# Kernel tuning notes

Hardware: AMD Instinct MI355X
Metric: run time of the kernel (lower is better)

The kernel has to match this reference:

```python
import jax, jax.numpy as jnp
import numpy as np

D = 1024
H = 16
HD = D // H
EPS = 1e-5

def _layernorm(x, g, b):
    xf = x.astype(jnp.float32)
    mu = jnp.mean(xf, axis=-1, keepdims=True)
    var = jnp.mean(jnp.square(xf - mu), axis=-1, keepdims=True)
    return ((xf - mu) * jax.lax.rsqrt(var + EPS) * g + b).astype(x.dtype)

def setup_inputs() -> dict:
    key = jax.random.key(0)
    ks = jax.random.split(key, 12)
    B, S = 4, 1024
    s_in = 1.0 / np.sqrt(D)
    inp = {
        "x": jax.random.normal(ks[0], (B, S, D), dtype=jnp.float32),
        "in_proj_w": jax.random.normal(ks[1], (3 * D, D), dtype=jnp.float32) * s_in,
        "in_proj_b": jnp.zeros((3 * D,), dtype=jnp.float32),
        "out_w": jax.random.normal(ks[2], (D, D), dtype=jnp.float32) * s_in,
        "out_b": jnp.zeros((D,), dtype=jnp.float32),
        "ln1_g": jnp.ones((D,), dtype=jnp.float32),
        "ln1_b": jnp.zeros((D,), dtype=jnp.float32),
        "fc_w": jax.random.normal(ks[3], (4 * D, D), dtype=jnp.float32) * s_in,
        "fc_b": jnp.zeros((4 * D,), dtype=jnp.float32),
        "proj_w": jax.random.normal(ks[4], (D, 4 * D), dtype=jnp.float32) * (1.0 / np.sqrt(4 * D)),
        "proj_b": jnp.zeros((D,), dtype=jnp.float32),
        "ln2_g": jnp.ones((D,), dtype=jnp.float32),
        "ln2_b": jnp.zeros((D,), dtype=jnp.float32),
    }
    return inp

def reference(x, in_proj_w, in_proj_b, out_w, out_b, ln1_g, ln1_b,
              fc_w, fc_b, proj_w, proj_b, ln2_g, ln2_b):
    B, S, _ = x.shape
    scaling = float(HD) ** -0.5
    # --- attention sublayer ---
    h = _layernorm(x, ln1_g, ln1_b)
    qkv = h @ in_proj_w.T + in_proj_b              # [B,S,3D]
    q, k, v = jnp.split(qkv, 3, axis=-1)
    q = (q * scaling).reshape(B, S, H, HD).transpose(0, 2, 1, 3)  # [B,H,S,hd]
    k = k.reshape(B, S, H, HD).transpose(0, 2, 1, 3)
    v = v.reshape(B, S, H, HD).transpose(0, 2, 1, 3)
    attn = jax.nn.softmax(jnp.einsum('bhqd,bhkd->bhqk', q, k), axis=-1)
    o = jnp.einsum('bhqk,bhkd->bhqd', attn, v).transpose(0, 2, 1, 3).reshape(B, S, D)
    x = x + o @ out_w.T + out_b
    # --- MLP sublayer (QuickGELU) ---
    h = _layernorm(x, ln2_g, ln2_b)
    u = h @ fc_w.T + fc_b                          # [B,S,4D]
    u = u * jax.nn.sigmoid(1.702 * u)
    x = x + u @ proj_w.T + proj_b
    return x
```

## Files before the change

### kernel.cpp

```cpp
#include <hip/hip_runtime.h>
#include <math.h>

#define D_MODEL 1024
#define SEQ     1024
#define BATCH   4
#define NTOK    (BATCH * SEQ)

typedef __bf16 bf16;
using bfrag  = __attribute__((ext_vector_type(8))) __bf16;
using ffrag  = __attribute__((ext_vector_type(4))) float;
using f32x16 = __attribute__((ext_vector_type(16))) float;

__device__ __forceinline__ ffrag mfma16(bfrag a, bfrag b, ffrag c) {
  return __builtin_amdgcn_mfma_f32_16x16x32_bf16(a, b, c, 0, 0, 0);
}
__device__ __forceinline__ f32x16 mfma32(bfrag a, bfrag b, f32x16 c) {
  return __builtin_amdgcn_mfma_f32_32x32x16_bf16(a, b, c, 0, 0, 0);
}
__device__ __forceinline__ unsigned cvt_pk(float lo, float hi) {
  unsigned r;
  asm("v_cvt_pk_bf16_f32 %0, %1, %2" : "=v"(r) : "v"(lo), "v"(hi));
  return r;
}

__device__ __forceinline__ void gload_lds16(const void* g, void* l) {
  __builtin_amdgcn_global_load_lds(
      (const __attribute__((address_space(1))) void*)g,
      (__attribute__((address_space(3))) void*)l, 16, 0, 0);
}

__device__ __forceinline__ int xcd_remap(int flat, int nwg) {
  return (flat & 7) * (nwg >> 3) + (flat >> 3);
}

__global__ void convert_all(const float* __restrict__ s0, bf16* __restrict__ d0, int n0,
                            const float* __restrict__ s1, bf16* __restrict__ d1, int n1,
                            const float* __restrict__ s2, bf16* __restrict__ d2, int n2,
                            const float* __restrict__ s3, bf16* __restrict__ d3, int n3,
                            float scale, int limit0) {
  const float* src; bf16* dst; int n; int limit = 0;
  switch (blockIdx.y) {
    case 0: src = s0; dst = d0; n = n0; limit = limit0; break;
    case 1: src = s1; dst = d1; n = n1; break;
    case 2: src = s2; dst = d2; n = n2; break;
    default: src = s3; dst = d3; n = n3; break;
  }
  int i = blockIdx.x * blockDim.x + threadIdx.x;
  const int stride = gridDim.x * blockDim.x;
  for (; i < n; i += stride) {
    float4 v = ((const float4*)src)[i];
    float sc = (i < limit) ? scale : 1.0f;
    bf16* d = dst + (size_t)i * 4;
    d[0] = (bf16)(v.x * sc); d[1] = (bf16)(v.y * sc);
    d[2] = (bf16)(v.z * sc); d[3] = (bf16)(v.w * sc);
  }
}

__global__ void scale_bias(const float* __restrict__ src, float* __restrict__ dst,
                           int n, int limit, float scale) {
  int i = blockIdx.x * blockDim.x + threadIdx.x;
  if (i < n) dst[i] = src[i] * (i < limit ? scale : 1.0f);
}

__global__ __launch_bounds__(256) void ln_row(const float* __restrict__ x,
                                              const float* __restrict__ gamma,
                                              const float* __restrict__ beta,
                                              bf16* __restrict__ out) {
  const int row = blockIdx.x, tid = threadIdx.x;
  const float4 v = ((const float4*)(x + (size_t)row * D_MODEL))[tid];
  float s  = v.x + v.y + v.z + v.w;
  float ss = v.x * v.x + v.y * v.y + v.z * v.z + v.w * v.w;
#pragma unroll
  for (int off = 32; off >= 1; off >>= 1) {
    s  += __shfl_xor(s, off);
    ss += __shfl_xor(ss, off);
  }
  __shared__ float rs[4], rss[4];
  const int w = tid >> 6;
  if ((tid & 63) == 0) { rs[w] = s; rss[w] = ss; }
  __syncthreads();
  s  = rs[0] + rs[1] + rs[2] + rs[3];
  ss = rss[0] + rss[1] + rss[2] + rss[3];
  const float mu   = s * (1.0f / D_MODEL);
  const float var  = ss * (1.0f / D_MODEL) - mu * mu;
  const float rstd = rsqrtf(var + 1e-5f);
  const float4 gv = ((const float4*)gamma)[tid];
  const float4 bv = ((const float4*)beta)[tid];
  bf16* o = out + (size_t)row * D_MODEL + tid * 4;
  o[0] = (bf16)((v.x - mu) * rstd * gv.x + bv.x);
  o[1] = (bf16)((v.y - mu) * rstd * gv.y + bv.y);
  o[2] = (bf16)((v.z - mu) * rstd * gv.z + bv.z);
  o[3] = (bf16)((v.w - mu) * rstd * gv.w + bv.w);
}

template <int EPI>
__global__ __launch_bounds__(256, 4) void gemm_bt(
    const bf16* __restrict__ A, const bf16* __restrict__ B,
    const float* __restrict__ bias, const float* __restrict__ resid,
    float* __restrict__ outF, bf16* __restrict__ outB,
    int M, int N, int K) {
  __shared__ bf16 As[2][128 * 32];
  __shared__ bf16 Bs[2][128 * 32];
  const int tid = threadIdx.x;
  const int lane = tid & 63, w = tid >> 6;
  const int wm = w >> 1, wn = w & 1;
  const int ql = lane & 15, lg = lane >> 4;
  const int nwg = gridDim.x * gridDim.y;
  const int flat = xcd_remap(blockIdx.y * gridDim.x + blockIdx.x, nwg);
  const int m0 = (flat % gridDim.x) * 128, n0 = (flat / gridDim.x) * 128;

  ffrag acc[4][4];
#pragma unroll
  for (int i = 0; i < 4; i++)
#pragma unroll
    for (int j = 0; j < 4; j++) acc[i][j] = ffrag{0.f, 0.f, 0.f, 0.f};

  const int r0 = tid >> 2;
  const int jsw = (tid & 3) ^ ((r0 >> 1) & 3);
  const bf16* a0 = A + (size_t)(m0 + r0) * K + jsw * 8;
  const bf16* a1 = A + (size_t)(m0 + 64 + r0) * K + jsw * 8;
  const bf16* b0 = B + (size_t)(n0 + r0) * K + jsw * 8;
  const bf16* b1 = B + (size_t)(n0 + 64 + r0) * K + jsw * 8;
  const int lo = w * 512;

  auto STAGE = [&](int bs, int kk) {
    gload_lds16(a0 + kk, &As[bs][lo]);
    gload_lds16(a1 + kk, &As[bs][2048 + lo]);
    gload_lds16(b0 + kk, &Bs[bs][lo]);
    gload_lds16(b1 + kk, &Bs[bs][2048 + lo]);
  };

  STAGE(0, 0);
  __syncthreads();

  int cur = 0;
  for (int k0 = 0; k0 < K; k0 += 32) {
    if (k0 + 32 < K) STAGE(cur ^ 1, k0 + 32);
    bfrag af[4], bfr[4];
#pragma unroll
    for (int i = 0; i < 4; i++) {
      const int row = wm * 64 + i * 16 + ql;
      af[i] = *(const bfrag*)&As[cur][row * 32 + ((lg ^ ((row >> 1) & 3)) * 8)];
    }
#pragma unroll
    for (int j = 0; j < 4; j++) {
      const int row = wn * 64 + j * 16 + ql;
      bfr[j] = *(const bfrag*)&Bs[cur][row * 32 + ((lg ^ ((row >> 1) & 3)) * 8)];
    }
#pragma unroll
    for (int i = 0; i < 4; i++)
#pragma unroll
      for (int j = 0; j < 4; j++)
        acc[i][j] = mfma16(af[i], bfr[j], acc[i][j]);
    __syncthreads();
    cur ^= 1;
  }

#pragma unroll
  for (int i = 0; i < 4; i++) {
    const int row = m0 + wm * 64 + i * 16 + lg * 4;
#pragma unroll
    for (int j = 0; j < 4; j++) {
      const int col = n0 + wn * 64 + j * 16 + ql;
      const float bv = bias[col];
#pragma unroll
      for (int r = 0; r < 4; r++) {
        float v = acc[i][j][r] + bv;
        const size_t idx = (size_t)(row + r) * N + col;
        if (EPI == 0) {
          outB[idx] = (bf16)v;
        } else if (EPI == 1) {
          outF[idx] = v + resid[idx];
        } else {
          outB[idx] = (bf16)(v / (1.0f + __expf(-1.702f * v)));
        }
      }
    }
  }
}

template <int EPI>
__global__ __launch_bounds__(256, 4) void gemm_bt64(
    const bf16* __restrict__ A, const bf16* __restrict__ B,
    const float* __restrict__ bias, const float* __restrict__ resid,
    float* __restrict__ outF, bf16* __restrict__ outB,
    int M, int N, int K) {
  __shared__ bf16 As[2][64 * 64];
  __shared__ bf16 Bs[2][64 * 64];
  const int tid = threadIdx.x;
  const int lane = tid & 63, w = tid >> 6;
  const int wm = w >> 1, wn = w & 1;
  const int ql = lane & 15, lg = lane >> 4;
  const int bid = blockIdx.x;
  const int k8 = bid & 7, j8 = bid >> 3;
  const int m0 = (k8 * 8 + (j8 & 7)) * 64;
  const int n0 = (j8 >> 3) * 64;

  ffrag acc[2][2];
#pragma unroll
  for (int i = 0; i < 2; i++)
#pragma unroll
    for (int j = 0; j < 2; j++) acc[i][j] = ffrag{0.f, 0.f, 0.f, 0.f};

  const int r0 = tid >> 3;
  const int jsw = ((tid & 7) ^ (r0 & 7)) * 8;
  const bf16* a0 = A + (size_t)(m0 + r0) * K + jsw;
  const bf16* a1 = A + (size_t)(m0 + 32 + r0) * K + jsw;
  const bf16* b0 = B + (size_t)(n0 + r0) * K + jsw;
  const bf16* b1 = B + (size_t)(n0 + 32 + r0) * K + jsw;
  const int lo = tid * 8;

  auto STAGE = [&](int bs, int kk) {
    gload_lds16(a0 + kk, &As[bs][lo]);
    gload_lds16(a1 + kk, &As[bs][2048 + lo]);
    gload_lds16(b0 + kk, &Bs[bs][lo]);
    gload_lds16(b1 + kk, &Bs[bs][2048 + lo]);
  };

  STAGE(0, 0);
  __syncthreads();

  int cur = 0;
  for (int k0 = 0; k0 < K; k0 += 64) {
    if (k0 + 64 < K) STAGE(cur ^ 1, k0 + 64);
    bfrag af[2][2], bfr[2][2];
#pragma unroll
    for (int i = 0; i < 2; i++) {
      const int row = wm * 32 + i * 16 + ql;
      const int r7 = row & 7;
#pragma unroll
      for (int kc = 0; kc < 2; kc++)
        af[i][kc] = *(const bfrag*)&As[cur][row * 64 + (((lg + 4 * kc) ^ r7) * 8)];
    }
#pragma unroll
    for (int j = 0; j < 2; j++) {
      const int row = wn * 32 + j * 16 + ql;
      const int r7 = row & 7;
#pragma unroll
      for (int kc = 0; kc < 2; kc++)
        bfr[j][kc] = *(const bfrag*)&Bs[cur][row * 64 + (((lg + 4 * kc) ^ r7) * 8)];
    }
#pragma unroll
    for (int kc = 0; kc < 2; kc++)
#pragma unroll
      for (int i = 0; i < 2; i++)
#pragma unroll
        for (int j = 0; j < 2; j++)
          acc[i][j] = mfma16(af[i][kc], bfr[j][kc], acc[i][j]);
    __syncthreads();
    cur ^= 1;
  }

#pragma unroll
  for (int i = 0; i < 2; i++) {
    const int row = m0 + wm * 32 + i * 16 + lg * 4;
#pragma unroll
    for (int j = 0; j < 2; j++) {
      const int col = n0 + wn * 32 + j * 16 + ql;
      const float bv = bias[col];
#pragma unroll
      for (int r = 0; r < 4; r++) {
        float v = acc[i][j][r] + bv;
        const size_t idx = (size_t)(row + r) * N + col;
        if (EPI == 0) {
          outB[idx] = (bf16)v;
        } else if (EPI == 1) {
          outF[idx] = v + resid[idx];
        } else {
          outB[idx] = (bf16)(v / (1.0f + __expf(-1.702f * v)));
        }
      }
    }
  }
}

__global__ __launch_bounds__(256) void transpose_v(const bf16* __restrict__ qkv,
                                                   bf16* __restrict__ vt) {
  __shared__ bf16 T[64 * 66];
  const int tid = threadIdx.x;
  const int bh = blockIdx.y, b = bh >> 4, h = bh & 15;
  const int s0 = blockIdx.x * 64;
  const bf16* src = qkv + (size_t)b * SEQ * 3072 + 2048 + h * 64;

  const int sl = tid >> 3, c = tid & 7;
#pragma unroll
  for (int p = 0; p < 2; p++) {
    const int s = sl + p * 32;
    const bfrag v = *(const bfrag*)(src + (size_t)(s0 + s) * 3072 + c * 8);
#pragma unroll
    for (int e = 0; e < 8; e++) T[s * 66 + c * 8 + e] = v[e];
  }
  __syncthreads();
  bf16* dst = vt + (size_t)bh * 64 * 1024;
#pragma unroll
  for (int p = 0; p < 2; p++) {
    const int d = sl + p * 32;
    bfrag o;
#pragma unroll
    for (int e = 0; e < 8; e++) o[e] = T[(c * 8 + e) * 66 + d];
    *(bfrag*)(dst + (size_t)d * 1024 + s0 + c * 8) = o;
  }
}

__global__ __launch_bounds__(256, 2) void flash_attn(const bf16* __restrict__ qkv,
                                                     const bf16* __restrict__ vt,
                                                     bf16* __restrict__ o) {
  __shared__ bf16 Kl[128 * 64];
  __shared__ bf16 Vl[64 * 128];
  __shared__ float RB[4][32];
  const int tid = threadIdx.x, lane = tid & 63, wid = tid >> 6;
  const int l31 = lane & 31, hi = lane >> 5;
  const int flat = xcd_remap(blockIdx.y * 8 + blockIdx.x, 512);
  const int qblk = flat & 7, bh = flat >> 3, b = bh >> 4, h = bh & 15;
  const int qb0 = qblk * 128 + wid * 32;
  const size_t headq = (size_t)b * SEQ * 3072 + (size_t)h * 64;

  const bf16* qp = qkv + headq + (size_t)(qb0 + l31) * 3072 + hi * 8;
  bfrag qb[4];
#pragma unroll
  for (int t = 0; t < 4; t++) qb[t] = *(const bfrag*)(qp + t * 16);

  float mrun = -1e30f, lrun = 0.0f;
  f32x16 oacc[2];
#pragma unroll
  for (int r = 0; r < 16; r++) { oacc[0][r] = 0.f; oacc[1][r] = 0.f; }

  const int ksrc = ((tid & 7) ^ ((tid >> 3) & 7) ^ wid) * 8;
  const bf16* kp = qkv + headq + 1024 + (size_t)(tid >> 3) * 3072 + ksrc;
  const bf16* vhead = vt + (size_t)bh * 64 * 1024;
  const int xlane = (l31 & 7) ^ (l31 >> 3);

  for (int kt = 0; kt < SEQ; kt += 128) {
#pragma unroll
    for (int pp = 0; pp < 4; pp++)
      gload_lds16(kp + (size_t)(kt + pp * 32) * 3072, &Kl[pp * 2048 + tid * 8]);
#pragma unroll
    for (int pp = 0; pp < 4; pp++) {
      const int vr = pp * 16 + (tid >> 4);
      const int gc = (tid & 15) ^ ((tid >> 4) & 7) ^ ((pp * 2 + (tid >> 7)) & 3);
      gload_lds16(vhead + (size_t)vr * 1024 + kt + gc * 8, &Vl[(pp * 256 + tid) * 8]);
    }
    __syncthreads();

    f32x16 sacc[4];
#pragma unroll
    for (int s = 0; s < 4; s++)
#pragma unroll
      for (int r = 0; r < 16; r++) sacc[s][r] = 0.f;
    __builtin_amdgcn_s_setprio(1);
#pragma unroll
    for (int s = 0; s < 4; s++) {
      const int krow = s * 32 + l31;
#pragma unroll
      for (int t = 0; t < 4; t++) {
        const int ch = (t * 2) ^ hi ^ xlane;
        const bfrag kf = *(const bfrag*)&Kl[krow * 64 + ch * 8];
        sacc[s] = mfma32(kf, qb[t], sacc[s]);
      }
    }
    __builtin_amdgcn_s_setprio(0);

    float lm = sacc[0][0];
#pragma unroll
    for (int s = 0; s < 4; s++)
#pragma unroll
      for (int r = 0; r < 16; r++) lm = fmaxf(lm, sacc[s][r]);

    if (!__all(lm - mrun <= 8.0f)) {
      const float mx = fmaxf(lm, __shfl_xor(lm, 32));
      const float mnew = fmaxf(mrun, mx);
      const float corr = exp2f(mrun - mnew);
      mrun = mnew;
      lrun *= corr;
      if (!hi) RB[wid][l31] = corr;
#pragma unroll
      for (int r = 0; r < 16; r++) {
        const float c = RB[wid][(r & 3) + 8 * (r >> 2) + 4 * hi];
        oacc[0][r] *= c;
        oacc[1][r] *= c;
      }
    }

#pragma unroll
    for (int s = 0; s < 4; s++) {
      float p[16];
#pragma unroll
      for (int r = 0; r < 16; r++) p[r] = exp2f(sacc[s][r] - mrun);
#pragma unroll
      for (int r = 0; r < 16; r++) lrun += p[r];
      const unsigned A = cvt_pk(p[0], p[1]),  B = cvt_pk(p[2], p[3]);
      const unsigned C = cvt_pk(p[4], p[5]),  D = cvt_pk(p[6], p[7]);
      const unsigned E = cvt_pk(p[8], p[9]),  F = cvt_pk(p[10], p[11]);
      const unsigned G = cvt_pk(p[12], p[13]), H = cvt_pk(p[14], p[15]);
      const unsigned x1 = __shfl_xor(hi ? A : C, 32);
      const unsigned x2 = __shfl_xor(hi ? B : D, 32);
      const unsigned x3 = __shfl_xor(hi ? E : G, 32);
      const unsigned x4 = __shfl_xor(hi ? F : H, 32);
      unsigned w0[4] = { hi ? x1 : A, hi ? x2 : B, hi ? C : x1, hi ? D : x2 };
      unsigned w1[4] = { hi ? x3 : E, hi ? x4 : F, hi ? G : x3, hi ? H : x4 };
      const bfrag pa0 = *(const bfrag*)w0;
      const bfrag pa1 = *(const bfrag*)w1;
      __builtin_amdgcn_s_setprio(1);
#pragma unroll
      for (int db = 0; db < 2; db++) {
        const int vrow = db * 32 + l31;
        const bfrag vf0 = *(const bfrag*)&Vl[vrow * 128 + ((((2 * s) * 2) ^ hi ^ xlane) & 15) * 8];
        oacc[db] = mfma32(pa0, vf0, oacc[db]);
        const bfrag vf1 = *(const bfrag*)&Vl[vrow * 128 + ((((2 * s + 1) * 2) ^ hi ^ xlane) & 15) * 8];
        oacc[db] = mfma32(pa1, vf1, oacc[db]);
      }
      __builtin_amdgcn_s_setprio(0);
    }
    __syncthreads();
  }

  const float lsum = lrun + __shfl_xor(lrun, 32);
  if (!hi) RB[wid][l31] = 1.0f / lsum;
#pragma unroll
  for (int r = 0; r < 16; r++) {
    const int qml = (r & 3) + 8 * (r >> 2) + 4 * hi;
    const float rv = RB[wid][qml];
    const size_t orow = (size_t)b * SEQ + qb0 + qml;
    o[orow * 1024 + h * 64 + l31]      = (bf16)(oacc[0][r] * rv);
    o[orow * 1024 + h * 64 + 32 + l31] = (bf16)(oacc[1][r] * rv);
  }
}

extern "C" void kernel_launch(void* const* d_in, const int* in_sizes, int n_in,
                              void* d_out, int out_size, void* d_ws, size_t ws_size,
                              hipStream_t stream) {
  (void)in_sizes; (void)n_in; (void)out_size; (void)ws_size;
  const float* x      = (const float*)d_in[0];
  const float* in_w   = (const float*)d_in[1];
  const float* in_b   = (const float*)d_in[2];
  const float* out_w  = (const float*)d_in[3];
  const float* out_b  = (const float*)d_in[4];
  const float* ln1_g  = (const float*)d_in[5];
  const float* ln1_b  = (const float*)d_in[6];
  const float* fc_w   = (const float*)d_in[7];
  const float* fc_b   = (const float*)d_in[8];
  const float* proj_w = (const float*)d_in[9];
  const float* proj_b = (const float*)d_in[10];
  const float* ln2_g  = (const float*)d_in[11];
  const float* ln2_b  = (const float*)d_in[12];
  float* out = (float*)d_out;

  char* p = (char*)d_ws;
  auto alloc = [&](size_t bytes) { char* r = p; p += (bytes + 255) & ~255ull; return r; };
  bf16* w_qkv  = (bf16*)alloc((size_t)3072 * 1024 * 2);
  bf16* w_out  = (bf16*)alloc((size_t)1024 * 1024 * 2);
  bf16* w_fc   = (bf16*)alloc((size_t)4096 * 1024 * 2);
  bf16* w_proj = (bf16*)alloc((size_t)1024 * 4096 * 2);
  float* b_qkv = (float*)alloc((size_t)3072 * 4);
  bf16* hbuf   = (bf16*)alloc((size_t)NTOK * 1024 * 2);
  float* x2    = (float*)alloc((size_t)NTOK * 1024 * 4);
  bf16* qkv    = (bf16*)alloc((size_t)NTOK * 3072 * 2);
  bf16* aout   = (bf16*)alloc((size_t)NTOK * 1024 * 2);
  bf16* ubuf   = qkv;
  bf16* vtb    = (bf16*)x2;

  const float scaling = 0.125f * 1.44269504089f;
  convert_all<<<dim3(1024, 4), 256, 0, stream>>>(
      in_w, w_qkv, 3072 * 1024 / 4,
      out_w, w_out, 1024 * 1024 / 4,
      fc_w, w_fc, 4096 * 1024 / 4,
      proj_w, w_proj, 4096 * 1024 / 4,
      scaling, 1024 * 1024 / 4);
  scale_bias<<<12, 256, 0, stream>>>(in_b, b_qkv, 3072, 1024, scaling);

  ln_row<<<NTOK, 256, 0, stream>>>(x, ln1_g, ln1_b, hbuf);
  gemm_bt<0><<<dim3(32, 24), 256, 0, stream>>>(hbuf, w_qkv, b_qkv, nullptr,
                                               nullptr, qkv, NTOK, 3072, 1024);
  transpose_v<<<dim3(16, 64), 256, 0, stream>>>(qkv, vtb);
  flash_attn<<<dim3(8, 64), 256, 0, stream>>>(qkv, vtb, aout);
  gemm_bt64<1><<<1024, 256, 0, stream>>>(aout, w_out, out_b, x,
                                         x2, nullptr, NTOK, 1024, 1024);
  ln_row<<<NTOK, 256, 0, stream>>>(x2, ln2_g, ln2_b, hbuf);
  gemm_bt<2><<<dim3(32, 32), 256, 0, stream>>>(hbuf, w_fc, fc_b, nullptr,
                                               nullptr, ubuf, NTOK, 4096, 1024);
  gemm_bt64<1><<<1024, 256, 0, stream>>>(ubuf, w_proj, proj_b, x2,
                                         out, nullptr, NTOK, 1024, 4096);
}
```

Before: 216.6 us.

## Fuse V transpose into QKV GEMM epilogue and split attention tile for occupancy

The QKV GEMM epilogue now writes the V columns directly in transposed [b,h,d,s] layout, which removes the separate transpose_v kernel and its extra read/write pass. The flash attention inner loop is split into two halves of 64 keys each, lowering live sacc registers, and the launch bound goes from 2 to 4 blocks per CU to raise occupancy. Doing the online-softmax rescale check twice per tile adds some overhead. The transposed epilogue writes 8-byte chunks strided by the sequence dimension, which may coalesce less well.

After: 219.5 us. About the same (+1.4%).

```diff
diff --git a/kernel.cpp b/kernel.cpp
--- a/kernel.cpp
+++ b/kernel.cpp
@@ -98,6 +98,7 @@
     const bf16* __restrict__ A, const bf16* __restrict__ B,
     const float* __restrict__ bias, const float* __restrict__ resid,
     float* __restrict__ outF, bf16* __restrict__ outB,
+    bf16* __restrict__ outV,
     int M, int N, int K) {
   __shared__ bf16 As[2][128 * 32];
   __shared__ bf16 Bs[2][128 * 32];
@@ -154,6 +155,26 @@
         acc[i][j] = mfma16(af[i], bfr[j], acc[i][j]);
     __syncthreads();
     cur ^= 1;
+  }
+
+  if (EPI == 0 && outV != nullptr && n0 >= 2048) {
+#pragma unroll
+    for (int i = 0; i < 4; i++) {
+      const int row = m0 + wm * 64 + i * 16 + lg * 4;
+      const int bb = row >> 10, ss = row & 1023;
+#pragma unroll
+      for (int j = 0; j < 4; j++) {
+        const int col = n0 + wn * 64 + j * 16 + ql;
+        const float bv = bias[col];
+        const int d = col - 2048, hh = d >> 6, dl = d & 63;
+        bf16 pk[4];
+#pragma unroll
+        for (int r = 0; r < 4; r++) pk[r] = (bf16)(acc[i][j][r] + bv);
+        *(uint2*)(outV + (((size_t)(bb * 16 + hh) * 64 + dl) * 1024 + ss)) =
+            *(const uint2*)pk;
+      }
+    }
+    return;
   }
 
 #pragma unroll
@@ -274,35 +295,7 @@
   }
 }
 
-__global__ __launch_bounds__(256) void transpose_v(const bf16* __restrict__ qkv,
-                                                   bf16* __restrict__ vt) {
-  __shared__ bf16 T[64 * 66];
-  const int tid = threadIdx.x;
-  const int bh = blockIdx.y, b = bh >> 4, h = bh & 15;
-  const int s0 = blockIdx.x * 64;
-  const bf16* src = qkv + (size_t)b * SEQ * 3072 + 2048 + h * 64;
-
-  const int sl = tid >> 3, c = tid & 7;
-#pragma unroll
-  for (int p = 0; p < 2; p++) {
-    const int s = sl + p * 32;
-    const bfrag v = *(const bfrag*)(src + (size_t)(s0 + s) * 3072 + c * 8);
-#pragma unroll
-    for (int e = 0; e < 8; e++) T[s * 66 + c * 8 + e] = v[e];
-  }
-  __syncthreads();
-  bf16* dst = vt + (size_t)bh * 64 * 1024;
-#pragma unroll
-  for (int p = 0; p < 2; p++) {
-    const int d = sl + p * 32;
-    bfrag o;
-#pragma unroll
-    for (int e = 0; e < 8; e++) o[e] = T[(c * 8 + e) * 66 + d];
-    *(bfrag*)(dst + (size_t)d * 1024 + s0 + c * 8) = o;
-  }
-}
-
-__global__ __launch_bounds__(256, 2) void flash_attn(const bf16* __restrict__ qkv,
+__global__ __launch_bounds__(256, 4) void flash_attn(const bf16* __restrict__ qkv,
                                                      const bf16* __restrict__ vt,
                                                      bf16* __restrict__ o) {
   __shared__ bf16 Kl[128 * 64];
@@ -342,74 +335,79 @@
     }
     __syncthreads();
 
-    f32x16 sacc[4];
-#pragma unroll
-    for (int s = 0; s < 4; s++)
-#pragma unroll
-      for (int r = 0; r < 16; r++) sacc[s][r] = 0.f;
-    __builtin_amdgcn_s_setprio(1);
-#pragma unroll
-    for (int s = 0; s < 4; s++) {
-      const int krow = s * 32 + l31;
-#pragma unroll
-      for (int t = 0; t < 4; t++) {
-        const int ch = (t * 2) ^ hi ^ xlane;
-        const bfrag kf = *(const bfrag*)&Kl[krow * 64 + ch * 8];
-        sacc[s] = mfma32(kf, qb[t], sacc[s]);
-      }
-    }
-    __builtin_amdgcn_s_setprio(0);
-
-    float lm = sacc[0][0];
-#pragma unroll
-    for (int s = 0; s < 4; s++)
-#pragma unroll
-      for (int r = 0; r < 16; r++) lm = fmaxf(lm, sacc[s][r]);
-
-    if (!__all(lm - mrun <= 8.0f)) {
-      const float mx = fmaxf(lm, __shfl_xor(lm, 32));
-      const float mnew = fmaxf(mrun, mx);
-      const float corr = exp2f(mrun - mnew);
-      mrun = mnew;
-      lrun *= corr;
-      if (!hi) RB[wid][l31] = corr;
-#pragma unroll
-      for (int r = 0; r < 16; r++) {
-        const float c = RB[wid][(r & 3) + 8 * (r >> 2) + 4 * hi];
-        oacc[0][r] *= c;
-        oacc[1][r] *= c;
-      }
-    }
-
-#pragma unroll
-    for (int s = 0; s < 4; s++) {
-      float p[16];
-#pragma unroll
-      for (int r = 0; r < 16; r++) p[r] = exp2f(sacc[s][r] - mrun);
-#pragma unroll
-      for (int r = 0; r < 16; r++) lrun += p[r];
-      const unsigned A = cvt_pk(p[0], p[1]),  B = cvt_pk(p[2], p[3]);
-      const unsigned C = cvt_pk(p[4], p[5]),  D = cvt_pk(p[6], p[7]);
-      const unsigned E = cvt_pk(p[8], p[9]),  F = cvt_pk(p[10], p[11]);
-      const unsigned G = cvt_pk(p[12], p[13]), H = cvt_pk(p[14], p[15]);
-      const unsigned x1 = __shfl_xor(hi ? A : C, 32);
-      const unsigned x2 = __shfl_xor(hi ? B : D, 32);
-      const unsigned x3 = __shfl_xor(hi ? E : G, 32);
-      const unsigned x4 = __shfl_xor(hi ? F : H, 32);
-      unsigned w0[4] = { hi ? x1 : A, hi ? x2 : B, hi ? C : x1, hi ? D : x2 };
-      unsigned w1[4] = { hi ? x3 : E, hi ? x4 : F, hi ? G : x3, hi ? H : x4 };
-      const bfrag pa0 = *(const bfrag*)w0;
-      const bfrag pa1 = *(const bfrag*)w1;
+#pragma unroll
+    for (int half = 0; half < 2; half++) {
+      f32x16 sacc[2];
+#pragma unroll
+      for (int s2 = 0; s2 < 2; s2++)
+#pragma unroll
+        for (int r = 0; r < 16; r++) sacc[s2][r] = 0.f;
       __builtin_amdgcn_s_setprio(1);
 #pragma unroll
-      for (int db = 0; db < 2; db++) {
-        const int vrow = db * 32 + l31;
-        const bfrag vf0 = *(const bfrag*)&Vl[vrow * 128 + ((((2 * s) * 2) ^ hi ^ xlane) & 15) * 8];
-        oacc[db] = mfma32(pa0, vf0, oacc[db]);
-        const bfrag vf1 = *(const bfrag*)&Vl[vrow * 128 + ((((2 * s + 1) * 2) ^ hi ^ xlane) & 15) * 8];
-        oacc[db] = mfma32(pa1, vf1, oacc[db]);
+      for (int s2 = 0; s2 < 2; s2++) {
+        const int krow = (half * 2 + s2) * 32 + l31;
+#pragma unroll
+        for (int t = 0; t < 4; t++) {
+          const int ch = (t * 2) ^ hi ^ xlane;
+          const bfrag kf = *(const bfrag*)&Kl[krow * 64 + ch * 8];
+          sacc[s2] = mfma32(kf, qb[t], sacc[s2]);
+        }
       }
       __builtin_amdgcn_s_setprio(0);
+
+      float lm = sacc[0][0];
+#pragma unroll
+      for (int s2 = 0; s2 < 2; s2++)
+#pragma unroll
+        for (int r = 0; r < 16; r++) lm = fmaxf(lm, sacc[s2][r]);
+
+      if (!__all(lm - mrun <= 8.0f)) {
+        const float mx = fmaxf(lm, __shfl_xor(lm, 32));
+        const float mnew = fmaxf(mrun, mx);
+        const float corr = exp2f(mrun - mnew);
+        mrun = mnew;
+        lrun *= corr;
+        if (!hi) RB[wid][l31] = corr;
+#pragma unroll
+        for (int r = 0; r < 16; r++) {
+          const float c = RB[wid][(r & 3) + 8 * (r >> 2) + 4 * hi];
+          oacc[0][r] *= c;
+          oacc[1][r] *= c;
+        }
+      }
+
+#pragma unroll
+      for (int s2 = 0; s2 < 2; s2++) {
+        const int s = half * 2 + s2;
+        auto pk2 = [&](int a, int bidx) {
+          const float ea = exp2f(sacc[s2][a] - mrun);
+          const float eb = exp2f(sacc[s2][bidx] - mrun);
+          lrun += ea + eb;
+          return cvt_pk(ea, eb);
+        };
+        const unsigned A = pk2(0, 1),   B = pk2(2, 3);
+        const unsigned C = pk2(4, 5),   D = pk2(6, 7);
+        const unsigned E = pk2(8, 9),   F = pk2(10, 11);
+        const unsigned G = pk2(12, 13), H = pk2(14, 15);
+        const unsigned x1 = __shfl_xor(hi ? A : C, 32);
+        const unsigned x2 = __shfl_xor(hi ? B : D, 32);
+        const unsigned x3 = __shfl_xor(hi ? E : G, 32);
+        const unsigned x4 = __shfl_xor(hi ? F : H, 32);
+        unsigned w0[4] = { hi ? x1 : A, hi ? x2 : B, hi ? C : x1, hi ? D : x2 };
+        unsigned w1[4] = { hi ? x3 : E, hi ? x4 : F, hi ? G : x3, hi ? H : x4 };
+        const bfrag pa0 = *(const bfrag*)w0;
+        const bfrag pa1 = *(const bfrag*)w1;
+        __builtin_amdgcn_s_setprio(1);
+#pragma unroll
+        for (int db = 0; db < 2; db++) {
+          const int vrow = db * 32 + l31;
+          const bfrag vf0 = *(const bfrag*)&Vl[vrow * 128 + ((((2 * s) * 2) ^ hi ^ xlane) & 15) * 8];
+          oacc[db] = mfma32(pa0, vf0, oacc[db]);
+          const bfrag vf1 = *(const bfrag*)&Vl[vrow * 128 + ((((2 * s + 1) * 2) ^ hi ^ xlane) & 15) * 8];
+          oacc[db] = mfma32(pa1, vf1, oacc[db]);
+        }
+        __builtin_amdgcn_s_setprio(0);
+      }
     }
     __syncthreads();
   }
@@ -470,14 +468,13 @@
 
   ln_row<<<NTOK, 256, 0, stream>>>(x, ln1_g, ln1_b, hbuf);
   gemm_bt<0><<<dim3(32, 24), 256, 0, stream>>>(hbuf, w_qkv, b_qkv, nullptr,
-                                               nullptr, qkv, NTOK, 3072, 1024);
-  transpose_v<<<dim3(16, 64), 256, 0, stream>>>(qkv, vtb);
+                                               nullptr, qkv, vtb, NTOK, 3072, 1024);
   flash_attn<<<dim3(8, 64), 256, 0, stream>>>(qkv, vtb, aout);
   gemm_bt64<1><<<1024, 256, 0, stream>>>(aout, w_out, out_b, x,
                                          x2, nullptr, NTOK, 1024, 1024);
   ln_row<<<NTOK, 256, 0, stream>>>(x2, ln2_g, ln2_b, hbuf);
   gemm_bt<2><<<dim3(32, 32), 256, 0, stream>>>(hbuf, w_fc, fc_b, nullptr,
-                                               nullptr, ubuf, NTOK, 4096, 1024);
+                                               nullptr, ubuf, nullptr, NTOK, 4096, 1024);
   gemm_bt64<1><<<1024, 256, 0, stream>>>(ubuf, w_proj, proj_b, x2,
                                          out, nullptr, NTOK, 1024, 4096);
 }
```
